# Optimization experiments

Measured on AMD Instinct MI355X. Metric: run time of the kernel, lower is better.

## Reference

```python
import jax, jax.numpy as jnp
import numpy as np

VOCAB = 50257
D_MODEL = 1024
RANK = 64
V1, V2 = 225, 224   # ceil(sqrt(vocab)), ceil(vocab/v1)
D1, D2 = 32, 32     # ceil(sqrt(d_model)), ceil(d_model/d1)
B, L = 4, 4096


def setup_inputs() -> dict:
    key = jax.random.key(0)
    ks = jax.random.split(key, 4)
    input_ids = jax.random.randint(ks[0], (B, L), 0, VOCAB, dtype=jnp.int32)
    core1_q = jax.random.randint(ks[1], (V1, 1, RANK, D1), -128, 128, dtype=jnp.int32).astype(jnp.int8)
    core2_q = jax.random.randint(ks[2], (V2, RANK, 1, D2), -128, 128, dtype=jnp.int32).astype(jnp.int8)
    phase_shift = jax.random.normal(ks[3], (RANK,), dtype=jnp.float32) * 0.02
    return {
        "input_ids": input_ids,
        "core1_q": core1_q,
        "core1_scale": jnp.float32(0.01),
        "core1_zp": jnp.float32(0.0),
        "core2_q": core2_q,
        "core2_scale": jnp.float32(0.01),
        "core2_zp": jnp.float32(0.0),
        "phase_shift": phase_shift,
    }


def reference(input_ids, core1_q, core1_scale, core1_zp, core2_q, core2_scale, core2_zp, phase_shift):
    # token index -> (row in core1, row in core2)
    idx1 = jnp.clip(input_ids // V2, 0, V1 - 1)  # [B, L]
    idx2 = jnp.clip(input_ids % V2, 0, V2 - 1)   # [B, L]

    # gather int8 rows first, then dequantize: (q - zp) * scale (same math as
    # dequantizing full cores then gathering, but avoids touching unused rows)
    c1 = (core1_q[idx1, 0].astype(jnp.float32) - core1_zp) * core1_scale     # [B, L, R, D1]
    c2 = (core2_q[idx2, :, 0].astype(jnp.float32) - core2_zp) * core2_scale  # [B, L, R, D2]

    # phase modulation on core1 along the rank axis
    c1 = c1 * jnp.cos(phase_shift)[None, None, :, None]

    # per-token rank contraction: [B,L,D1,D2] -> [B,L,D1*D2] -> slice d_model
    out = jnp.einsum('blrd,blrf->bldf', c1, c2).reshape(B, L, D1 * D2)
    return out[:, :, :D_MODEL]
```

## Files before the change

kernel.cpp:

```cpp
#include <hip/hip_runtime.h>
#include <hip/hip_bf16.h>
#include <math.h>

#define V1N   225
#define V2N   224
#define RANK  64
#define DDIM  32
#define ROWE  (RANK*DDIM)

typedef __bf16  bf16x8 __attribute__((ext_vector_type(8)));
typedef float  f32x16 __attribute__((ext_vector_type(16)));
typedef float  f32x4  __attribute__((ext_vector_type(4)));
typedef int    i32x4  __attribute__((ext_vector_type(4)));

__global__ __launch_bounds__(256) void prep_tables(
    const int* __restrict__ c1q, const int* __restrict__ c2q,
    const float* __restrict__ s1p, const float* __restrict__ z1p,
    const float* __restrict__ s2p, const float* __restrict__ z2p,
    const float* __restrict__ phase,
    __bf16* __restrict__ t1, __bf16* __restrict__ t2)
{
    __shared__ float lds[64 * 33];
    __shared__ float cosv[RANK];

    int v = blockIdx.x;
    bool is1 = (v < V1N);
    const int* src;
    __bf16* dst;
    float sc, zp;
    if (is1) { src = c1q + v * ROWE;            dst = t1 + (size_t)v * ROWE;  sc = *s1p; zp = *z1p; }
    else     { int u = v - V1N; src = c2q + u * ROWE; dst = t2 + (size_t)u * ROWE; sc = *s2p; zp = *z2p; }

    int t = threadIdx.x;
    if (is1 && t < RANK) cosv[t] = cosf(phase[t]);
    __syncthreads();

    i32x4 w0 = reinterpret_cast<const i32x4*>(src)[t * 2];
    i32x4 w1 = reinterpret_cast<const i32x4*>(src)[t * 2 + 1];
    #pragma unroll
    for (int j = 0; j < 8; ++j) {
        int e = t * 8 + j;
        int q = (j < 4) ? w0[j & 3] : w1[j & 3];
        float val = ((float)q - zp) * sc;
        if (is1) val *= cosv[e >> 5];
        lds[(e >> 5) * 33 + (e & 31)] = val;
    }
    __syncthreads();

    int s   = t >> 6;
    int d   = (t >> 1) & 31;
    int rr0 = (t & 1) * 8;
    bf16x8 o8;
    #pragma unroll
    for (int j = 0; j < 8; ++j) {
        int r = s * 16 + rr0 + j;
        o8[j] = (__bf16)lds[r * 33 + d];
    }
    *reinterpret_cast<bf16x8*>(dst + t * 8) = o8;
}

__global__ __launch_bounds__(256) void tt_main(
    const int* __restrict__ ids,
    const __bf16* __restrict__ t1, const __bf16* __restrict__ t2,
    float* __restrict__ out, int n_tok)
{
    __shared__ float tile[4][32 * 33];

    int w    = threadIdx.x >> 6;
    int wave = (blockIdx.x << 2) + w;
    int lane = threadIdx.x & 63;
    int m = lane & 31;
    int g = lane >> 5;
    bool active = (wave < n_tok);

    if (active) {
        unsigned id = (unsigned)ids[wave];
        unsigned i1 = id / 224u; if (i1 > (unsigned)(V1N - 1)) i1 = V1N - 1;
        unsigned i2 = id % 224u;

        const __bf16* a_base = t2 + (size_t)i2 * ROWE + m * 16 + g * 8;
        const __bf16* b_base = t1 + (size_t)i1 * ROWE + m * 16 + g * 8;

        f32x16 acc;
        #pragma unroll
        for (int i = 0; i < 16; ++i) acc[i] = 0.0f;

        #pragma unroll
        for (int s = 0; s < 4; ++s) {
            bf16x8 a = *reinterpret_cast<const bf16x8*>(a_base + s * 512);
            bf16x8 b = *reinterpret_cast<const bf16x8*>(b_base + s * 512);
            acc = __builtin_amdgcn_mfma_f32_32x32x16_bf16(a, b, acc, 0, 0, 0);
        }

        float* tp = tile[w];
        #pragma unroll
        for (int q = 0; q < 4; ++q) {
            #pragma unroll
            for (int j = 0; j < 4; ++j) {
                tp[m * 33 + 8 * q + 4 * g + j] = acc[4 * q + j];
            }
        }
    }
    __syncthreads();
    if (active) {
        const float* tp = tile[w];
        float* o = out + (size_t)wave * 1024;
        #pragma unroll
        for (int p = 0; p < 4; ++p) {
            int d1 = p * 8 + (lane >> 3);
            int d2 = (lane & 7) * 4;
            f32x4 v = { tp[d1 * 33 + d2 + 0], tp[d1 * 33 + d2 + 1],
                        tp[d1 * 33 + d2 + 2], tp[d1 * 33 + d2 + 3] };
            *reinterpret_cast<f32x4*>(o + p * 256 + lane * 4) = v;
        }
    }
}

__global__ __launch_bounds__(256) void tt_fused(
    const int* __restrict__ ids,
    const int* __restrict__ c1q, const int* __restrict__ c2q,
    const float* __restrict__ s1p, const float* __restrict__ z1p,
    const float* __restrict__ s2p, const float* __restrict__ z2p,
    const float* __restrict__ phase,
    float* __restrict__ out, int n_tok)
{
    __shared__ float cosv[RANK];
    if (threadIdx.x < RANK) cosv[threadIdx.x] = cosf(phase[threadIdx.x]);
    __syncthreads();

    int wave = (blockIdx.x << 2) + (threadIdx.x >> 6);
    if (wave >= n_tok) return;
    int lane = threadIdx.x & 63;
    int m = lane & 31;
    int g = lane >> 5;

    float s1 = *s1p, z1 = *z1p, s2 = *s2p, z2 = *z2p;

    unsigned id = (unsigned)ids[wave];
    unsigned i1 = id / 224u; if (i1 > (unsigned)(V1N - 1)) i1 = V1N - 1;
    unsigned i2 = id % 224u;

    const int* a_src = c2q + (size_t)i2 * ROWE + m;
    const int* b_src = c1q + (size_t)i1 * ROWE + m;

    f32x16 acc;
    #pragma unroll
    for (int i = 0; i < 16; ++i) acc[i] = 0.0f;

    #pragma unroll
    for (int s = 0; s < 4; ++s) {
        bf16x8 a, b;
        #pragma unroll
        for (int j = 0; j < 8; ++j) {
            int r = s * 16 + g * 8 + j;
            a[j] = (__bf16)((((float)a_src[r * 32]) - z2) * s2);
            b[j] = (__bf16)((((float)b_src[r * 32]) - z1) * s1 * cosv[r]);
        }
        acc = __builtin_amdgcn_mfma_f32_32x32x16_bf16(a, b, acc, 0, 0, 0);
    }

    float* o = out + (size_t)wave * 1024 + m * 32 + g * 4;
    #pragma unroll
    for (int q = 0; q < 4; ++q) {
        f32x4 v = { acc[4 * q + 0], acc[4 * q + 1], acc[4 * q + 2], acc[4 * q + 3] };
        *reinterpret_cast<f32x4*>(o + 8 * q) = v;
    }
}

extern "C" void kernel_launch(void* const* d_in, const int* in_sizes, int n_in,
                              void* d_out, int out_size, void* d_ws, size_t ws_size,
                              hipStream_t stream) {
    const int*   ids = (const int*)d_in[0];
    const int*   c1q = (const int*)d_in[1];
    const float* s1  = (const float*)d_in[2];
    const float* z1  = (const float*)d_in[3];
    const int*   c2q = (const int*)d_in[4];
    const float* s2  = (const float*)d_in[5];
    const float* z2  = (const float*)d_in[6];
    const float* ph  = (const float*)d_in[7];
    float* out = (float*)d_out;

    int n_tok = in_sizes[0];
    int grid  = (n_tok + 3) / 4;

    size_t need = (size_t)(V1N + V2N) * ROWE * sizeof(__bf16);
    if (ws_size >= need) {
        __bf16* t1 = (__bf16*)d_ws;
        __bf16* t2 = t1 + (size_t)V1N * ROWE;
        prep_tables<<<V1N + V2N, 256, 0, stream>>>(c1q, c2q, s1, z1, s2, z2, ph, t1, t2);
        tt_main<<<grid, 256, 0, stream>>>(ids, t1, t2, out, n_tok);
    } else {
        tt_fused<<<grid, 256, 0, stream>>>(ids, c1q, c2q, s1, z1, s2, z2, ph, out, n_tok);
    }
}
```

Baseline: 24.65 us.

## Process two tokens per wave and one table row per wave in prep

The main kernel now has each wave handle two tokens, issuing all table loads for both before the MFMAs so more memory requests are in flight. It also drops the block-wide barrier, since each wave only uses its own LDS tile. The prep kernel now maps one table row per wave instead of per block, giving a quarter as many blocks and wave-local transposes without a second barrier. This doubles register and LDS use per wave and halves the number of waves in the main grid, which may reduce latency hiding.

```diff
diff --git a/kernel.cpp b/kernel.cpp
--- a/kernel.cpp
+++ b/kernel.cpp
@@ -20,43 +20,49 @@
     const float* __restrict__ phase,
     __bf16* __restrict__ t1, __bf16* __restrict__ t2)
 {
-    __shared__ float lds[64 * 33];
     __shared__ float cosv[RANK];
-
-    int v = blockIdx.x;
+    __shared__ float lds[4][64 * 33];
+
+    int t = threadIdx.x;
+    if (t < RANK) cosv[t] = cosf(phase[t]);
+    __syncthreads();
+
+    int w    = t >> 6;
+    int lane = t & 63;
+    int v    = blockIdx.x * 4 + w;
+    if (v >= V1N + V2N) return;
+
     bool is1 = (v < V1N);
-    const int* src;
-    __bf16* dst;
-    float sc, zp;
-    if (is1) { src = c1q + v * ROWE;            dst = t1 + (size_t)v * ROWE;  sc = *s1p; zp = *z1p; }
-    else     { int u = v - V1N; src = c2q + u * ROWE; dst = t2 + (size_t)u * ROWE; sc = *s2p; zp = *z2p; }
-
-    int t = threadIdx.x;
-    if (is1 && t < RANK) cosv[t] = cosf(phase[t]);
-    __syncthreads();
-
-    i32x4 w0 = reinterpret_cast<const i32x4*>(src)[t * 2];
-    i32x4 w1 = reinterpret_cast<const i32x4*>(src)[t * 2 + 1];
-    #pragma unroll
-    for (int j = 0; j < 8; ++j) {
-        int e = t * 8 + j;
-        int q = (j < 4) ? w0[j & 3] : w1[j & 3];
-        float val = ((float)q - zp) * sc;
-        if (is1) val *= cosv[e >> 5];
-        lds[(e >> 5) * 33 + (e & 31)] = val;
-    }
-    __syncthreads();
-
-    int s   = t >> 6;
-    int d   = (t >> 1) & 31;
-    int rr0 = (t & 1) * 8;
-    bf16x8 o8;
-    #pragma unroll
-    for (int j = 0; j < 8; ++j) {
-        int r = s * 16 + rr0 + j;
-        o8[j] = (__bf16)lds[r * 33 + d];
-    }
-    *reinterpret_cast<bf16x8*>(dst + t * 8) = o8;
+    const int* src; __bf16* dst; float sc, zp;
+    if (is1) { src = c1q + (size_t)v * ROWE;            dst = t1 + (size_t)v * ROWE;  sc = *s1p; zp = *z1p; }
+    else     { int u = v - V1N; src = c2q + (size_t)u * ROWE; dst = t2 + (size_t)u * ROWE; sc = *s2p; zp = *z2p; }
+
+    float* L = lds[w];
+    #pragma unroll
+    for (int p = 0; p < 4; ++p) {
+        i32x4 q0 = reinterpret_cast<const i32x4*>(src)[p * 128 + lane * 2];
+        i32x4 q1 = reinterpret_cast<const i32x4*>(src)[p * 128 + lane * 2 + 1];
+        #pragma unroll
+        for (int j = 0; j < 8; ++j) {
+            int e = p * 512 + lane * 8 + j;
+            int q = (j < 4) ? q0[j & 3] : q1[j & 3];
+            float val = ((float)q - zp) * sc;
+            if (is1) val *= cosv[e >> 5];
+            L[(e >> 5) * 33 + (e & 31)] = val;
+        }
+    }
+    #pragma unroll
+    for (int h = 0; h < 4; ++h) {
+        int d   = lane >> 1;
+        int rr0 = (lane & 1) * 8;
+        bf16x8 o8;
+        #pragma unroll
+        for (int j = 0; j < 8; ++j) {
+            int r = h * 16 + rr0 + j;
+            o8[j] = (__bf16)L[r * 33 + d];
+        }
+        *reinterpret_cast<bf16x8*>(dst + h * 512 + lane * 8) = o8;
+    }
 }
 
 __global__ __launch_bounds__(256) void tt_main(
@@ -64,47 +70,86 @@
     const __bf16* __restrict__ t1, const __bf16* __restrict__ t2,
     float* __restrict__ out, int n_tok)
 {
-    __shared__ float tile[4][32 * 33];
+    __shared__ float tile[4][2][32 * 33];
 
     int w    = threadIdx.x >> 6;
-    int wave = (blockIdx.x << 2) + w;
     int lane = threadIdx.x & 63;
     int m = lane & 31;
     int g = lane >> 5;
-    bool active = (wave < n_tok);
-
-    if (active) {
-        unsigned id = (unsigned)ids[wave];
+    int tok0 = ((blockIdx.x << 2) + w) * 2;
+    int tok1 = tok0 + 1;
+    bool act0 = (tok0 < n_tok);
+    bool act1 = (tok1 < n_tok);
+
+    bf16x8 a0[4], b0[4], a1[4], b1[4];
+
+    if (act0) {
+        unsigned id = (unsigned)ids[tok0];
         unsigned i1 = id / 224u; if (i1 > (unsigned)(V1N - 1)) i1 = V1N - 1;
         unsigned i2 = id % 224u;
-
-        const __bf16* a_base = t2 + (size_t)i2 * ROWE + m * 16 + g * 8;
-        const __bf16* b_base = t1 + (size_t)i1 * ROWE + m * 16 + g * 8;
-
+        const __bf16* ab = t2 + (size_t)i2 * ROWE + m * 16 + g * 8;
+        const __bf16* bb = t1 + (size_t)i1 * ROWE + m * 16 + g * 8;
+        #pragma unroll
+        for (int s = 0; s < 4; ++s) {
+            a0[s] = *reinterpret_cast<const bf16x8*>(ab + s * 512);
+            b0[s] = *reinterpret_cast<const bf16x8*>(bb + s * 512);
+        }
+    }
+    if (act1) {
+        unsigned id = (unsigned)ids[tok1];
+        unsigned i1 = id / 224u; if (i1 > (unsigned)(V1N - 1)) i1 = V1N - 1;
+        unsigned i2 = id % 224u;
+        const __bf16* ab = t2 + (size_t)i2 * ROWE + m * 16 + g * 8;
+        const __bf16* bb = t1 + (size_t)i1 * ROWE + m * 16 + g * 8;
+        #pragma unroll
+        for (int s = 0; s < 4; ++s) {
+            a1[s] = *reinterpret_cast<const bf16x8*>(ab + s * 512);
+            b1[s] = *reinterpret_cast<const bf16x8*>(bb + s * 512);
+        }
+    }
+
+    if (act0) {
         f32x16 acc;
         #pragma unroll
         for (int i = 0; i < 16; ++i) acc[i] = 0.0f;
-
-        #pragma unroll
-        for (int s = 0; s < 4; ++s) {
-            bf16x8 a = *reinterpret_cast<const bf16x8*>(a_base + s * 512);
-            bf16x8 b = *reinterpret_cast<const bf16x8*>(b_base + s * 512);
-            acc = __builtin_amdgcn_mfma_f32_32x32x16_bf16(a, b, acc, 0, 0, 0);
-        }
-
-        float* tp = tile[w];
-        #pragma unroll
-        for (int q = 0; q < 4; ++q) {
+        #pragma unroll
+        for (int s = 0; s < 4; ++s)
+            acc = __builtin_amdgcn_mfma_f32_32x32x16_bf16(a0[s], b0[s], acc, 0, 0, 0);
+
+        float* tp = tile[w][0];
+        #pragma unroll
+        for (int q = 0; q < 4; ++q)
             #pragma unroll
-            for (int j = 0; j < 4; ++j) {
+            for (int j = 0; j < 4; ++j)
                 tp[m * 33 + 8 * q + 4 * g + j] = acc[4 * q + j];
-            }
-        }
-    }
-    __syncthreads();
-    if (active) {
-        const float* tp = tile[w];
-        float* o = out + (size_t)wave * 1024;
+
+        float* o = out + (size_t)tok0 * 1024;
+        #pragma unroll
+        for (int p = 0; p < 4; ++p) {
+            int d1 = p * 8 + (lane >> 3);
+            int d2 = (lane & 7) * 4;
+            f32x4 v = { tp[d1 * 33 + d2 + 0], tp[d1 * 33 + d2 + 1],
+                        tp[d1 * 33 + d2 + 2], tp[d1 * 33 + d2 + 3] };
+            *reinterpret_cast<f32x4*>(o + p * 256 + lane * 4) = v;
+        }
+    }
+
+    if (act1) {
+        f32x16 acc;
+        #pragma unroll
+        for (int i = 0; i < 16; ++i) acc[i] = 0.0f;
+        #pragma unroll
+        for (int s = 0; s < 4; ++s)
+            acc = __builtin_amdgcn_mfma_f32_32x32x16_bf16(a1[s], b1[s], acc, 0, 0, 0);
+
+        float* tp = tile[w][1];
+        #pragma unroll
+        for (int q = 0; q < 4; ++q)
+            #pragma unroll
+            for (int j = 0; j < 4; ++j)
+                tp[m * 33 + 8 * q + 4 * g + j] = acc[4 * q + j];
+
+        float* o = out + (size_t)tok1 * 1024;
         #pragma unroll
         for (int p = 0; p < 4; ++p) {
             int d1 = p * 8 + (lane >> 3);
@@ -181,15 +226,16 @@
     float* out = (float*)d_out;
 
     int n_tok = in_sizes[0];
-    int grid  = (n_tok + 3) / 4;
+    int grid  = (n_tok + 7) / 8;
 
     size_t need = (size_t)(V1N + V2N) * ROWE * sizeof(__bf16);
     if (ws_size >= need) {
         __bf16* t1 = (__bf16*)d_ws;
         __bf16* t2 = t1 + (size_t)V1N * ROWE;
-        prep_tables<<<V1N + V2N, 256, 0, stream>>>(c1q, c2q, s1, z1, s2, z2, ph, t1, t2);
+        prep_tables<<<(V1N + V2N + 3) / 4, 256, 0, stream>>>(c1q, c2q, s1, z1, s2, z2, ph, t1, t2);
         tt_main<<<grid, 256, 0, stream>>>(ids, t1, t2, out, n_tok);
     } else {
-        tt_fused<<<grid, 256, 0, stream>>>(ids, c1q, c2q, s1, z1, s2, z2, ph, out, n_tok);
-    }
-}
+        int fgrid = (n_tok + 3) / 4;
+        tt_fused<<<fgrid, 256, 0, stream>>>(ids, c1q, c2q, s1, z1, s2, z2, ph, out, n_tok);
+    }
+}
```

Measured after the change: 26.07 us. +5.8%, slower.
